# Kernel tuning notes

Hardware: AMD Instinct MI355X
Metric: run time of the kernel (lower is better)

Reference implementation:

```python
import jax, jax.numpy as jnp
import numpy as np
from jax import lax

L, H, NUM_CONVS, KSIZE = 8192, 128, 4, 7
EPS = 1e-5


def _pos_encoding(length, dim, dtype):
    pos = jnp.arange(length, dtype=jnp.float32)[:, None]
    i = jnp.arange(dim, dtype=jnp.float32)[None, :]
    angle = pos / jnp.power(10000.0, (2.0 * jnp.floor(i / 2.0)) / dim)
    pe = jnp.where((jnp.arange(dim) % 2 == 0)[None, :], jnp.sin(angle), jnp.cos(angle))
    return pe.astype(dtype)


def _layer_norm(x):
    mu = jnp.mean(x, axis=-1, keepdims=True)
    var = jnp.mean(jnp.square(x - mu), axis=-1, keepdims=True)
    return (x - mu) * lax.rsqrt(var + EPS)


def _conv1d_same(x, w, b):
    # x: [L, H]; w: [H_out, H_in, K]; b: [H_out]. SAME padding over sequence.
    lhs = x.T[None]  # [1, H, L]
    out = lax.conv_general_dilated(lhs, w, window_strides=(1,), padding='SAME',
                                   dimension_numbers=('NCH', 'OIH', 'NCH'))
    return (out[0] + b[:, None]).T  # [L, H]


def setup_inputs() -> dict:
    key = jax.random.key(0)
    ks = jax.random.split(key, 12)
    s = 0.02
    return {
        'x': jax.random.normal(ks[0], (L, H), jnp.float32),
        'conv_w': jax.random.normal(ks[1], (NUM_CONVS, H, H, KSIZE), jnp.float32) * s,
        'conv_b': jax.random.normal(ks[2], (NUM_CONVS, H), jnp.float32) * s,
        'Wq': jax.random.normal(ks[3], (H, H), jnp.float32) * s,
        'bq': jax.random.normal(ks[4], (H,), jnp.float32) * s,
        'Wk': jax.random.normal(ks[5], (H, H), jnp.float32) * s,
        'bk': jax.random.normal(ks[6], (H,), jnp.float32) * s,
        'Wv': jax.random.normal(ks[7], (H, H), jnp.float32) * s,
        'bv': jax.random.normal(ks[8], (H,), jnp.float32) * s,
        'Wff': jax.random.normal(ks[9], (H, H), jnp.float32) * s,
        'bff': jax.random.normal(ks[10], (H,), jnp.float32) * s,
    }


def reference(x, conv_w, conv_b, Wq, bq, Wk, bk, Wv, bv, Wff, bff):
    h = x + _pos_encoding(x.shape[0], x.shape[1], x.dtype)
    # conv stack: LN -> conv -> residual, repeated num_convs times
    for i in range(NUM_CONVS):
        residual = h
        h = _conv1d_same(_layer_norm(h), conv_w[i], conv_b[i]) + residual
    # self-attention (single-head as written in the source)
    residual = h
    n = _layer_norm(h)
    q = n @ Wq.T + bq
    k = n @ Wk.T + bk
    v = n @ Wv.T + bv
    scale = 1.0 / jnp.sqrt(jnp.asarray(H, h.dtype))
    attn = jax.nn.softmax((q @ k.T) * scale, axis=-1)  # [L, L]
    h = attn @ v + residual
    # feed-forward
    residual = h
    h = jax.nn.relu(_layer_norm(h) @ Wff.T + bff) + residual
    return h
```

## Files before the change

kernel.cpp:

```cpp
#include <hip/hip_runtime.h>

#define LL 8192
#define HH 128

typedef __attribute__((ext_vector_type(8))) short short8v;
typedef __attribute__((ext_vector_type(4))) short short4v;
typedef __attribute__((ext_vector_type(4))) float f32x4;
typedef __attribute__((ext_vector_type(16))) float f32x16;

__device__ inline short f2bf(float f) {
    union { float f; unsigned u; } x; x.f = f;
    unsigned r = (x.u + 0x7fffu + ((x.u >> 16) & 1u)) >> 16;
    return (short)r;
}
__device__ inline float bf2f(short s) {
    union { unsigned u; float f; } x; x.u = ((unsigned)(unsigned short)s) << 16;
    return x.f;
}

__device__ inline float fexp2(float x) {
#if defined(__has_builtin)
#if __has_builtin(__builtin_amdgcn_exp2f)
    return __builtin_amdgcn_exp2f(x);
#else
    return __expf(x * 0.6931471805599453f);
#endif
#else
    return __expf(x * 0.6931471805599453f);
#endif
}

__device__ inline unsigned pack_hi16(unsigned hi, unsigned lo) {
#if defined(__has_builtin)
#if __has_builtin(__builtin_amdgcn_perm)
    return __builtin_amdgcn_perm(hi, lo, 0x07060302u);
#endif
#endif
    return (lo >> 16) | (hi & 0xffff0000u);
}

__device__ inline void plane32swap(unsigned& a, unsigned& b) {
#if defined(__has_builtin)
#if __has_builtin(__builtin_amdgcn_permlane32_swap)
    typedef unsigned u2v __attribute__((ext_vector_type(2)));
    u2v r = __builtin_amdgcn_permlane32_swap(a, b, false, false);
    a = r[0]; b = r[1];
    return;
#endif
#endif
    asm volatile("v_permlane32_swap_b32 %0, %1" : "+v"(a), "+v"(b));
}

__device__ inline short* sAp(short* base, int row, int col) {
    int byte = (row << 8) + (col << 1);
    byte ^= (row & 7) << 4;
    return (short*)((char*)base + byte);
}

__device__ inline short8v ln_pack8(const float* rowF, int l15) {
    const float4 a = *(const float4*)&rowF[l15 * 8];
    const float4 b = *(const float4*)&rowF[l15 * 8 + 4];
    float s  = (a.x + a.y) + (a.z + a.w) + (b.x + b.y) + (b.z + b.w);
    float s2 = a.x * a.x + a.y * a.y + a.z * a.z + a.w * a.w
             + b.x * b.x + b.y * b.y + b.z * b.z + b.w * b.w;
#pragma unroll
    for (int off = 1; off <= 8; off <<= 1) {
        s  += __shfl_xor(s,  off, 64);
        s2 += __shfl_xor(s2, off, 64);
    }
    float mu = s * (1.f / 128.f);
    float var = s2 * (1.f / 128.f) - mu * mu;
    float rstd = rsqrtf(var + 1e-5f);
    short8v r;
    r[0] = f2bf((a.x - mu) * rstd);
    r[1] = f2bf((a.y - mu) * rstd);
    r[2] = f2bf((a.z - mu) * rstd);
    r[3] = f2bf((a.w - mu) * rstd);
    r[4] = f2bf((b.x - mu) * rstd);
    r[5] = f2bf((b.y - mu) * rstd);
    r[6] = f2bf((b.z - mu) * rstd);
    r[7] = f2bf((b.w - mu) * rstd);
    return r;
}

__global__ __launch_bounds__(256) void repack_all(const float* __restrict__ x,
                                                  const float* __restrict__ w,
                                                  const float* __restrict__ Wq,
                                                  const float* __restrict__ Wk,
                                                  const float* __restrict__ Wv,
                                                  const float* __restrict__ bq,
                                                  const float* __restrict__ bk,
                                                  const float* __restrict__ bv,
                                                  const float* __restrict__ Wff,
                                                  short* __restrict__ wkb,
                                                  short* __restrict__ wqkvb,
                                                  float* __restrict__ b3,
                                                  short* __restrict__ wffb,
                                                  float* __restrict__ h0) {
    const float qs = 0.08838834764831845f * 1.4426950408889634f;
    int idx = blockIdx.x * 256 + threadIdx.x;
    if (idx < 458752) {
        int k = idx % 7;
        int t = idx / 7;
        int i = t % HH; t /= HH;
        int o = t % HH;
        int lay = t / HH;
        wkb[((lay * 7 + k) * HH + o) * HH + i] = f2bf(w[idx]);
    } else {
        int j = idx - 458752;
        if (j < 49152) {
            int t = j >> 14, r = j & 16383;
            float v = (t == 0) ? Wq[r] * qs : (t == 1) ? Wk[r] : Wv[r];
            wqkvb[j] = f2bf(v);
        } else if (j < 49536) {
            int jj = j - 49152;
            b3[jj] = (jj < 128) ? bq[jj] * qs : (jj < 256) ? bk[jj - 128] : bv[jj - 256];
        } else if (j < 65920) {
            int jj = j - 49536;
            wffb[jj] = f2bf(Wff[jj]);
        } else {
            int p = j - 65920;
            if (p < 262144) {
                int g = p >> 5, c4 = (p & 31) << 2;
                float4 val = *(const float4*)&x[g * HH + c4];
                float fg = (float)g;
#pragma unroll
                for (int h = 0; h < 2; h++) {
                    int i0 = c4 + h * 2;
                    float e = (float)i0 / 128.f;
                    float ang = fg / powf(10000.f, e);
                    ((float*)&val)[h * 2]     += sinf(ang);
                    ((float*)&val)[h * 2 + 1] += cosf(ang);
                }
                *(float4*)&h0[g * HH + c4] = val;
            }
        }
    }
}

__global__ __launch_bounds__(256, 4) void conv_layer_kernel(const float* __restrict__ hin,
                                                            const short* __restrict__ wkb,
                                                            const float* __restrict__ conv_b,
                                                            float* __restrict__ hout,
                                                            int lay) {
    __shared__ float sF[22][132];
    __shared__ short sA[22 * 128];
    int tid = threadIdx.x;
    int w = tid >> 6, lane = tid & 63;
    int l15 = lane & 15, quad = lane >> 4;
    int wg = blockIdx.x;
    int m0 = ((wg & 7) * 64 + (wg >> 4)) * 16;
    int c0w = (((wg >> 3) & 1)) * 64 + w * 16;

    for (int idx = tid; idx < 22 * 32; idx += 256) {
        int r = idx >> 5, c4 = (idx & 31) << 2;
        int g = m0 - 3 + r;
        float4 val = make_float4(0.f, 0.f, 0.f, 0.f);
        if (g >= 0 && g < LL) val = *(const float4*)&hin[g * HH + c4];
        *(float4*)&sF[r][c4] = val;
    }
    __syncthreads();
#pragma unroll
    for (int rr = 0; rr < 2; rr++) {
        int row = rr * 16 + w * 4 + quad;
        if (row < 22)
            *(short8v*)sAp(sA, row, l15 * 8) = ln_pack8(&sF[row][0], l15);
    }
    __syncthreads();
    f32x4 accA = (f32x4)(0.f), accB = (f32x4)(0.f);
    const short* wl = wkb + lay * 7 * HH * HH;
    for (int k = 0; k < 7; k++) {
        const short* b0 = wl + (k * HH + c0w + l15) * HH;
#pragma unroll
        for (int ks = 0; ks < 4; ks++) {
            short8v bf = *(const short8v*)&b0[ks * 32 + quad * 8];
            short8v af = *(const short8v*)sAp(sA, l15 + k, ks * 32 + quad * 8);
            if (ks & 1) accB = __builtin_amdgcn_mfma_f32_16x16x32_bf16(af, bf, accB, 0, 0, 0);
            else        accA = __builtin_amdgcn_mfma_f32_16x16x32_bf16(af, bf, accA, 0, 0, 0);
        }
    }
    float bb = conv_b[lay * HH + c0w + l15];
#pragma unroll
    for (int r = 0; r < 4; r++) {
        int row = quad * 4 + r;
        hout[(m0 + row) * HH + c0w + l15] =
            sF[3 + row][c0w + l15] + accA[r] + accB[r] + bb;
    }
}

__global__ __launch_bounds__(256, 2) void conv_qkv_kernel(const float* __restrict__ hin,
                                                          const short* __restrict__ wkb,
                                                          const float* __restrict__ conv_b,
                                                          const short* __restrict__ wqkvb,
                                                          const float* __restrict__ b3,
                                                          float* __restrict__ hB,
                                                          short* __restrict__ qb,
                                                          short* __restrict__ kb,
                                                          short* __restrict__ vt) {
    __shared__ float sF[22][132];
    __shared__ short sA[22 * 128];
    __shared__ short sT[4][32][17];
    int tid = threadIdx.x;
    int w = tid >> 6, lane = tid & 63;
    int l15 = lane & 15, quad = lane >> 4;
    int wg = blockIdx.x;
    int m0 = ((wg & 7) * 64 + (wg >> 3)) * 16;
    int c0 = w * 32;

    for (int idx = tid; idx < 22 * 32; idx += 256) {
        int r = idx >> 5, c4 = (idx & 31) << 2;
        int g = m0 - 3 + r;
        float4 val = make_float4(0.f, 0.f, 0.f, 0.f);
        if (g >= 0 && g < LL) val = *(const float4*)&hin[g * HH + c4];
        *(float4*)&sF[r][c4] = val;
    }
    __syncthreads();
#pragma unroll
    for (int rr = 0; rr < 2; rr++) {
        int row = rr * 16 + w * 4 + quad;
        if (row < 22)
            *(short8v*)sAp(sA, row, l15 * 8) = ln_pack8(&sF[row][0], l15);
    }
    __syncthreads();
    f32x4 a0 = (f32x4)(0.f), a1 = (f32x4)(0.f);
    const short* wl = wkb + 3 * 7 * HH * HH;
    for (int k = 0; k < 7; k++) {
        const short* b0 = wl + (k * HH + c0 + l15) * HH;
        const short* b1 = b0 + 16 * HH;
#pragma unroll
        for (int ks = 0; ks < 4; ks++) {
            short8v bf0 = *(const short8v*)&b0[ks * 32 + quad * 8];
            short8v bf1 = *(const short8v*)&b1[ks * 32 + quad * 8];
            short8v af = *(const short8v*)sAp(sA, l15 + k, ks * 32 + quad * 8);
            a0 = __builtin_amdgcn_mfma_f32_16x16x32_bf16(af, bf0, a0, 0, 0, 0);
            a1 = __builtin_amdgcn_mfma_f32_16x16x32_bf16(af, bf1, a1, 0, 0, 0);
        }
    }
    float bb0 = conv_b[3 * HH + c0 + l15], bb1 = conv_b[3 * HH + c0 + 16 + l15];
#pragma unroll
    for (int r = 0; r < 4; r++) {
        int row = quad * 4 + r;
        float v0 = sF[3 + row][c0 + l15]      + a0[r] + bb0;
        float v1 = sF[3 + row][c0 + 16 + l15] + a1[r] + bb1;
        sF[3 + row][c0 + l15]      = v0;
        sF[3 + row][c0 + 16 + l15] = v1;
        hB[(m0 + row) * HH + c0 + l15]      = v0;
        hB[(m0 + row) * HH + c0 + 16 + l15] = v1;
    }
    __syncthreads();
    {
        int row = w * 4 + quad;
        *(short8v*)sAp(sA, row, l15 * 8) = ln_pack8(&sF[3 + row][0], l15);
    }
    __syncthreads();
    short8v af4[4];
#pragma unroll
    for (int ks = 0; ks < 4; ks++)
        af4[ks] = *(const short8v*)sAp(sA, l15, ks * 32 + quad * 8);

    for (int t = 0; t < 3; t++) {
        f32x4 acc0 = (f32x4)(0.f), acc1 = (f32x4)(0.f);
        const short* b0 = wqkvb + (t * 128 + c0 + l15) * HH;
        const short* b1 = b0 + 16 * HH;
#pragma unroll
        for (int ks = 0; ks < 4; ks++) {
            short8v bf0 = *(const short8v*)&b0[ks * 32 + quad * 8];
            short8v bf1 = *(const short8v*)&b1[ks * 32 + quad * 8];
            acc0 = __builtin_amdgcn_mfma_f32_16x16x32_bf16(af4[ks], bf0, acc0, 0, 0, 0);
            acc1 = __builtin_amdgcn_mfma_f32_16x16x32_bf16(af4[ks], bf1, acc1, 0, 0, 0);
        }
        float qb0 = b3[t * 128 + c0 + l15], qb1 = b3[t * 128 + c0 + 16 + l15];
        if (t < 2) {
            short* o = (t == 0) ? qb : kb;
#pragma unroll
            for (int r = 0; r < 4; r++) {
                int lr = m0 + quad * 4 + r;
                o[lr * HH + c0 + l15]      = f2bf(acc0[r] + qb0);
                o[lr * HH + c0 + 16 + l15] = f2bf(acc1[r] + qb1);
            }
        } else {
#pragma unroll
            for (int r = 0; r < 4; r++) {
                sT[w][l15][quad * 4 + r]      = f2bf(acc0[r] + qb0);
                sT[w][16 + l15][quad * 4 + r] = f2bf(acc1[r] + qb1);
            }
            asm volatile("s_waitcnt lgkmcnt(0)" ::: "memory");
#pragma unroll
            for (int cc = 0; cc < 8; cc++) {
                int col = cc * 4 + quad;
                vt[(c0 + col) * LL + m0 + l15] = sT[w][col][l15];
            }
        }
    }
}

#define FBN 64

__global__ __launch_bounds__(256, 2) void flash_mfma_kernel(const short* __restrict__ qs,
                                                            const short* __restrict__ ksrc,
                                                            const short* __restrict__ vsrc,
                                                            short* __restrict__ PO,
                                                            float* __restrict__ Pl,
                                                            int segrows) {
    __shared__ short sK[16 * 64 * 8];
    __shared__ short sV[16 * 64 * 8];

    const int tid = threadIdx.x;
    const int w = tid >> 6, lane = tid & 63;
    const int l31 = lane & 31, hi = lane >> 5;
    const int seg = blockIdx.x & 7;
    const int m0 = (blockIdx.x >> 3) * 128;
    const int jbeg = seg * segrows;
    const int nchunk = segrows >> 6;
    const int qrow = m0 + w * 32 + l31;

    short8v qf[8];
#pragma unroll
    for (int ks = 0; ks < 8; ks++)
        qf[ks] = *(const short8v*)&qs[qrow * HH + ks * 16 + hi * 8];

    float l_r = 0.f;
    f32x16 o_acc[4];
#pragma unroll
    for (int dt = 0; dt < 4; dt++) o_acc[dt] = (f32x16)(0.f);

    short8v kr[4], vr[4];
#pragma unroll
    for (int r = 0; r < 4; r++) {
        int s = w + 4 * r;
        kr[r] = *(const short8v*)&ksrc[(jbeg + (s >> 3) * 32 + l31) * HH + (s & 7) * 16 + hi * 8];
        vr[r] = *(const short8v*)&vsrc[((s >> 2) * 32 + l31) * LL + jbeg + (s & 3) * 16 + hi * 8];
    }

    for (int c = 0; c < nchunk; c++) {
        __syncthreads();
#pragma unroll
        for (int r = 0; r < 4; r++) {
            int s = w + 4 * r;
            *(short8v*)&sK[(s * 64 + lane) * 8] = kr[r];
            *(short8v*)&sV[(s * 64 + lane) * 8] = vr[r];
        }
        __syncthreads();
        if (c + 1 < nchunk) {
            const int j1 = jbeg + (c + 1) * FBN;
#pragma unroll
            for (int r = 0; r < 4; r++) {
                int s = w + 4 * r;
                kr[r] = *(const short8v*)&ksrc[(j1 + (s >> 3) * 32 + l31) * HH + (s & 7) * 16 + hi * 8];
                vr[r] = *(const short8v*)&vsrc[((s >> 2) * 32 + l31) * LL + j1 + (s & 3) * 16 + hi * 8];
            }
        }
        f32x16 s0 = (f32x16)(0.f), s1 = (f32x16)(0.f);
        __builtin_amdgcn_s_setprio(1);
#pragma unroll
        for (int ks = 0; ks < 8; ks++) {
            short8v kf0 = *(const short8v*)&sK[((ks) * 64 + lane) * 8];
            short8v kf1 = *(const short8v*)&sK[((8 + ks) * 64 + lane) * 8];
            s0 = __builtin_amdgcn_mfma_f32_32x32x16_bf16(kf0, qf[ks], s0, 0, 0, 0);
            s1 = __builtin_amdgcn_mfma_f32_32x32x16_bf16(kf1, qf[ks], s1, 0, 0, 0);
        }
        __builtin_amdgcn_s_setprio(0);
        short8v pfrag[4];
#pragma unroll
        for (int nt = 0; nt < 2; nt++) {
            const f32x16& sa = nt ? s1 : s0;
            unsigned pw[8];
#pragma unroll
            for (int m = 0; m < 8; m++) {
                float p0 = fexp2(sa[2 * m]);
                float p1 = fexp2(sa[2 * m + 1]);
                l_r += p0 + p1;
                union { float f; unsigned u; } u0, u1;
                u0.f = p0; u1.f = p1;
                pw[m] = pack_hi16(u1.u, u0.u);
            }
            plane32swap(pw[0], pw[2]);
            plane32swap(pw[1], pw[3]);
            plane32swap(pw[4], pw[6]);
            plane32swap(pw[5], pw[7]);
            union { unsigned u[4]; short8v v; } fa, fb;
            fa.u[0] = pw[0]; fa.u[1] = pw[1]; fa.u[2] = pw[2]; fa.u[3] = pw[3];
            fb.u[0] = pw[4]; fb.u[1] = pw[5]; fb.u[2] = pw[6]; fb.u[3] = pw[7];
            pfrag[nt * 2]     = fa.v;
            pfrag[nt * 2 + 1] = fb.v;
        }
        __builtin_amdgcn_s_setprio(1);
#pragma unroll
        for (int ks = 0; ks < 4; ks++)
#pragma unroll
            for (int dt = 0; dt < 4; dt++) {
                short8v vf = *(const short8v*)&sV[((dt * 4 + ks) * 64 + lane) * 8];
                o_acc[dt] = __builtin_amdgcn_mfma_f32_32x32x16_bf16(pfrag[ks], vf, o_acc[dt], 0, 0, 0);
            }
        __builtin_amdgcn_s_setprio(0);
    }
    float lsum = l_r + __shfl_xor(l_r, 32, 64);
    if (hi == 0)
        Pl[seg * LL + qrow] = lsum;
#pragma unroll
    for (int dt = 0; dt < 4; dt++)
#pragma unroll
        for (int i = 0; i < 16; i++) {
            int qr = (i & 3) + 8 * (i >> 2) + 4 * hi;
            PO[(size_t)seg * LL * HH + (size_t)(m0 + w * 32 + qr) * HH + dt * 32 + l31] =
                f2bf(o_acc[dt][i]);
        }
}

__global__ __launch_bounds__(256) void ff_kernel(const float* __restrict__ hin,
                                                 const short* __restrict__ PO,
                                                 const float* __restrict__ Pl,
                                                 const short* __restrict__ wffb,
                                                 const float* __restrict__ bff,
                                                 float* __restrict__ out,
                                                 int nsplit) {
    __shared__ float sF[16][132];
    __shared__ short sA[16 * 128];
    __shared__ float sLi[16];
    int tid = threadIdx.x;
    int w = tid >> 6, lane = tid & 63;
    int l15 = lane & 15, quad = lane >> 4;
    int wg = blockIdx.x;
    int m0 = ((wg & 7) * 64 + (wg >> 3)) * 16;

    if (tid < 16) {
        float s = 0.f;
        for (int seg = 0; seg < nsplit; seg++) s += Pl[seg * LL + m0 + tid];
        sLi[tid] = 1.f / s;
    }
    __syncthreads();
    for (int idx = tid; idx < 16 * 32; idx += 256) {
        int r = idx >> 5, c4 = (idx & 31) << 2;
        float4 hv = *(const float4*)&hin[(m0 + r) * HH + c4];
        float s0 = 0.f, s1 = 0.f, s2 = 0.f, s3 = 0.f;
        for (int seg = 0; seg < nsplit; seg++) {
            short4v pv = *(const short4v*)&PO[(size_t)seg * LL * HH + (m0 + r) * HH + c4];
            s0 += bf2f(pv[0]); s1 += bf2f(pv[1]); s2 += bf2f(pv[2]); s3 += bf2f(pv[3]);
        }
        float li = sLi[r];
        *(float4*)&sF[r][c4] = make_float4(hv.x + s0 * li, hv.y + s1 * li,
                                           hv.z + s2 * li, hv.w + s3 * li);
    }
    __syncthreads();
    {
        int row = w * 4 + quad;
        *(short8v*)sAp(sA, row, l15 * 8) = ln_pack8(&sF[row][0], l15);
    }
    __syncthreads();
    int c0 = w * 32;
    f32x4 acc0 = (f32x4)(0.f), acc1 = (f32x4)(0.f);
    const short* b0 = wffb + (c0 + l15) * HH;
    const short* b1 = b0 + 16 * HH;
#pragma unroll
    for (int ks = 0; ks < 4; ks++) {
        short8v af = *(const short8v*)sAp(sA, l15, ks * 32 + quad * 8);
        short8v bf0 = *(const short8v*)&b0[ks * 32 + quad * 8];
        short8v bf1 = *(const short8v*)&b1[ks * 32 + quad * 8];
        acc0 = __builtin_amdgcn_mfma_f32_16x16x32_bf16(af, bf0, acc0, 0, 0, 0);
        acc1 = __builtin_amdgcn_mfma_f32_16x16x32_bf16(af, bf1, acc1, 0, 0, 0);
    }
    float bb0 = bff[c0 + l15], bb1 = bff[c0 + 16 + l15];
#pragma unroll
    for (int r = 0; r < 4; r++) {
        int lr = quad * 4 + r;
        out[(m0 + lr) * HH + c0 + l15]      = fmaxf(acc0[r] + bb0, 0.f) + sF[lr][c0 + l15];
        out[(m0 + lr) * HH + c0 + 16 + l15] = fmaxf(acc1[r] + bb1, 0.f) + sF[lr][c0 + 16 + l15];
    }
}

extern "C" void kernel_launch(void* const* d_in, const int* in_sizes, int n_in,
                              void* d_out, int out_size, void* d_ws, size_t ws_size,
                              hipStream_t stream) {
    const float* x      = (const float*)d_in[0];
    const float* conv_w = (const float*)d_in[1];
    const float* conv_b = (const float*)d_in[2];
    const float* Wq = (const float*)d_in[3];
    const float* bq = (const float*)d_in[4];
    const float* Wk = (const float*)d_in[5];
    const float* bk = (const float*)d_in[6];
    const float* Wv = (const float*)d_in[7];
    const float* bv = (const float*)d_in[8];
    const float* Wff = (const float*)d_in[9];
    const float* bff = (const float*)d_in[10];
    float* out = (float*)d_out;

    char* ws = (char*)d_ws;
    const size_t MB = 1u << 20;
    float* hB   = (float*)(ws);
    short* qb   = (short*)(ws + 4 * MB);
    short* kb   = (short*)(ws + 6 * MB);
    short* vt   = (short*)(ws + 8 * MB);
    float* Pl   = (float*)(ws + 10 * MB);
    short* wffb = (short*)(ws + 10 * MB + 524288);
    short* PO   = (short*)(ws + 10 * MB + 524288 + 32768);
    short* wkb   = (short*)(ws + 16 * MB);
    short* wqkvb = (short*)(ws + 17 * MB);
    float* b3    = (float*)(ws + 17 * MB + 131072);
    float* h0    = (float*)(ws + 18 * MB);
    float* h13   = (float*)(ws + 22 * MB);
    float* h2    = h0;

    const int nsplit = 8;
    const int segrows = LL / nsplit;

    repack_all<<<3074, 256, 0, stream>>>(x, conv_w, Wq, Wk, Wv, bq, bk, bv, Wff,
                                         wkb, wqkvb, b3, wffb, h0);
    conv_layer_kernel<<<LL / 16 * 2, 256, 0, stream>>>(h0,  wkb, conv_b, h13, 0);
    conv_layer_kernel<<<LL / 16 * 2, 256, 0, stream>>>(h13, wkb, conv_b, h2,  1);
    conv_layer_kernel<<<LL / 16 * 2, 256, 0, stream>>>(h2,  wkb, conv_b, h13, 2);
    conv_qkv_kernel<<<LL / 16, 256, 0, stream>>>(h13, wkb, conv_b, wqkvb, b3,
                                                 hB, qb, kb, vt);
    flash_mfma_kernel<<<LL / 128 * nsplit, 256, 0, stream>>>(qb, kb, vt, PO, Pl, segrows);
    ff_kernel<<<LL / 16, 256, 0, stream>>>(hB, PO, Pl, wffb, bff, out, nsplit);
}
```

Before: 205.8 us.

## Fuse conv layers pairwise with halo recompute and widen attention split to sixteen

Each conv kernel now does two conv layers per block. It loads a 6-row halo and recomputes the intermediate rows for the second layer in shared memory, so the launches and global round-trips for layers 1 and 3 go away. The flash kernel's split count becomes a parameter and rises to 16 when the workspace is large enough, with segments mapped per XCD. The ff kernel is templated on the split count so its reduction loops unroll. The cost is extra MFMA work on the halo, more shared memory per block, and more partial outputs to reduce.

```diff
diff --git a/kernel.cpp b/kernel.cpp
--- a/kernel.cpp
+++ b/kernel.cpp
@@ -138,23 +138,23 @@
     }
 }
 
-__global__ __launch_bounds__(256, 4) void conv_layer_kernel(const float* __restrict__ hin,
-                                                            const short* __restrict__ wkb,
-                                                            const float* __restrict__ conv_b,
-                                                            float* __restrict__ hout,
-                                                            int lay) {
-    __shared__ float sF[22][132];
-    __shared__ short sA[22 * 128];
+__global__ __launch_bounds__(256, 2) void conv2_kernel(const float* __restrict__ hin,
+                                                       const short* __restrict__ wkb,
+                                                       const float* __restrict__ conv_b,
+                                                       float* __restrict__ hout,
+                                                       int lay0) {
+    __shared__ float sF[28][132];
+    __shared__ short sA[28 * 128];
     int tid = threadIdx.x;
     int w = tid >> 6, lane = tid & 63;
     int l15 = lane & 15, quad = lane >> 4;
     int wg = blockIdx.x;
-    int m0 = ((wg & 7) * 64 + (wg >> 4)) * 16;
-    int c0w = (((wg >> 3) & 1)) * 64 + w * 16;
-
-    for (int idx = tid; idx < 22 * 32; idx += 256) {
+    int m0 = ((wg & 7) * 64 + (wg >> 3)) * 16;
+    int c0 = w * 32;
+
+    for (int idx = tid; idx < 28 * 32; idx += 256) {
         int r = idx >> 5, c4 = (idx & 31) << 2;
-        int g = m0 - 3 + r;
+        int g = m0 - 6 + r;
         float4 val = make_float4(0.f, 0.f, 0.f, 0.f);
         if (g >= 0 && g < LL) val = *(const float4*)&hin[g * HH + c4];
         *(float4*)&sF[r][c4] = val;
@@ -163,42 +163,86 @@
 #pragma unroll
     for (int rr = 0; rr < 2; rr++) {
         int row = rr * 16 + w * 4 + quad;
-        if (row < 22)
+        if (row < 28)
             *(short8v*)sAp(sA, row, l15 * 8) = ln_pack8(&sF[row][0], l15);
     }
     __syncthreads();
-    f32x4 accA = (f32x4)(0.f), accB = (f32x4)(0.f);
-    const short* wl = wkb + lay * 7 * HH * HH;
+    const short* wl0 = wkb + lay0 * 7 * HH * HH;
+    f32x4 t0a = (f32x4)(0.f), t0b = (f32x4)(0.f);
+    f32x4 t1a = (f32x4)(0.f), t1b = (f32x4)(0.f);
     for (int k = 0; k < 7; k++) {
-        const short* b0 = wl + (k * HH + c0w + l15) * HH;
+        const short* bw0 = wl0 + (k * HH + c0 + l15) * HH;
+        const short* bw1 = bw0 + 16 * HH;
 #pragma unroll
         for (int ks = 0; ks < 4; ks++) {
-            short8v bf = *(const short8v*)&b0[ks * 32 + quad * 8];
-            short8v af = *(const short8v*)sAp(sA, l15 + k, ks * 32 + quad * 8);
-            if (ks & 1) accB = __builtin_amdgcn_mfma_f32_16x16x32_bf16(af, bf, accB, 0, 0, 0);
-            else        accA = __builtin_amdgcn_mfma_f32_16x16x32_bf16(af, bf, accA, 0, 0, 0);
-        }
-    }
-    float bb = conv_b[lay * HH + c0w + l15];
+            short8v bf0 = *(const short8v*)&bw0[ks * 32 + quad * 8];
+            short8v bf1 = *(const short8v*)&bw1[ks * 32 + quad * 8];
+            short8v a0 = *(const short8v*)sAp(sA, l15 + k, ks * 32 + quad * 8);
+            short8v a1 = *(const short8v*)sAp(sA, 6 + l15 + k, ks * 32 + quad * 8);
+            t0a = __builtin_amdgcn_mfma_f32_16x16x32_bf16(a0, bf0, t0a, 0, 0, 0);
+            t0b = __builtin_amdgcn_mfma_f32_16x16x32_bf16(a0, bf1, t0b, 0, 0, 0);
+            t1a = __builtin_amdgcn_mfma_f32_16x16x32_bf16(a1, bf0, t1a, 0, 0, 0);
+            t1b = __builtin_amdgcn_mfma_f32_16x16x32_bf16(a1, bf1, t1b, 0, 0, 0);
+        }
+    }
+    float b0l = conv_b[lay0 * HH + c0 + l15], b0h = conv_b[lay0 * HH + c0 + 16 + l15];
 #pragma unroll
     for (int r = 0; r < 4; r++) {
-        int row = quad * 4 + r;
-        hout[(m0 + row) * HH + c0w + l15] =
-            sF[3 + row][c0w + l15] + accA[r] + accB[r] + bb;
-    }
-}
-
-__global__ __launch_bounds__(256, 2) void conv_qkv_kernel(const float* __restrict__ hin,
-                                                          const short* __restrict__ wkb,
-                                                          const float* __restrict__ conv_b,
-                                                          const short* __restrict__ wqkvb,
-                                                          const float* __restrict__ b3,
-                                                          float* __restrict__ hB,
-                                                          short* __restrict__ qb,
-                                                          short* __restrict__ kb,
-                                                          short* __restrict__ vt) {
-    __shared__ float sF[22][132];
-    __shared__ short sA[22 * 128];
+        int rr0 = quad * 4 + r;
+        sF[3 + rr0][c0 + l15]      += t0a[r] + b0l;
+        sF[3 + rr0][c0 + 16 + l15] += t0b[r] + b0h;
+        if (rr0 >= 10) {
+            sF[9 + rr0][c0 + l15]      += t1a[r] + b0l;
+            sF[9 + rr0][c0 + 16 + l15] += t1b[r] + b0h;
+        }
+    }
+    __syncthreads();
+#pragma unroll
+    for (int rr = 0; rr < 2; rr++) {
+        int row = 3 + rr * 16 + w * 4 + quad;
+        if (row < 25) {
+            short8v pk = ln_pack8(&sF[row][0], l15);
+            int g = m0 - 6 + row;
+            if (g < 0 || g >= LL) pk = (short8v)(short)0;
+            *(short8v*)sAp(sA, row, l15 * 8) = pk;
+        }
+    }
+    __syncthreads();
+    const short* wl1 = wkb + (lay0 + 1) * 7 * HH * HH;
+    f32x4 ca = (f32x4)(0.f), cb = (f32x4)(0.f);
+    for (int k = 0; k < 7; k++) {
+        const short* bw0 = wl1 + (k * HH + c0 + l15) * HH;
+        const short* bw1 = bw0 + 16 * HH;
+#pragma unroll
+        for (int ks = 0; ks < 4; ks++) {
+            short8v bf0 = *(const short8v*)&bw0[ks * 32 + quad * 8];
+            short8v bf1 = *(const short8v*)&bw1[ks * 32 + quad * 8];
+            short8v af = *(const short8v*)sAp(sA, 3 + l15 + k, ks * 32 + quad * 8);
+            ca = __builtin_amdgcn_mfma_f32_16x16x32_bf16(af, bf0, ca, 0, 0, 0);
+            cb = __builtin_amdgcn_mfma_f32_16x16x32_bf16(af, bf1, cb, 0, 0, 0);
+        }
+    }
+    float b1l = conv_b[(lay0 + 1) * HH + c0 + l15], b1h = conv_b[(lay0 + 1) * HH + c0 + 16 + l15];
+#pragma unroll
+    for (int r = 0; r < 4; r++) {
+        int i = 6 + quad * 4 + r;
+        int g = m0 + quad * 4 + r;
+        hout[g * HH + c0 + l15]      = sF[i][c0 + l15]      + ca[r] + b1l;
+        hout[g * HH + c0 + 16 + l15] = sF[i][c0 + 16 + l15] + cb[r] + b1h;
+    }
+}
+
+__global__ __launch_bounds__(256, 2) void conv2_qkv_kernel(const float* __restrict__ hin,
+                                                           const short* __restrict__ wkb,
+                                                           const float* __restrict__ conv_b,
+                                                           const short* __restrict__ wqkvb,
+                                                           const float* __restrict__ b3,
+                                                           float* __restrict__ hB,
+                                                           short* __restrict__ qb,
+                                                           short* __restrict__ kb,
+                                                           short* __restrict__ vt) {
+    __shared__ float sF[28][132];
+    __shared__ short sA[28 * 128];
     __shared__ short sT[4][32][17];
     int tid = threadIdx.x;
     int w = tid >> 6, lane = tid & 63;
@@ -207,9 +251,9 @@
     int m0 = ((wg & 7) * 64 + (wg >> 3)) * 16;
     int c0 = w * 32;
 
-    for (int idx = tid; idx < 22 * 32; idx += 256) {
+    for (int idx = tid; idx < 28 * 32; idx += 256) {
         int r = idx >> 5, c4 = (idx & 31) << 2;
-        int g = m0 - 3 + r;
+        int g = m0 - 6 + r;
         float4 val = make_float4(0.f, 0.f, 0.f, 0.f);
         if (g >= 0 && g < LL) val = *(const float4*)&hin[g * HH + c4];
         *(float4*)&sF[r][c4] = val;
@@ -218,39 +262,81 @@
 #pragma unroll
     for (int rr = 0; rr < 2; rr++) {
         int row = rr * 16 + w * 4 + quad;
-        if (row < 22)
+        if (row < 28)
             *(short8v*)sAp(sA, row, l15 * 8) = ln_pack8(&sF[row][0], l15);
     }
     __syncthreads();
-    f32x4 a0 = (f32x4)(0.f), a1 = (f32x4)(0.f);
-    const short* wl = wkb + 3 * 7 * HH * HH;
+    const short* wl2 = wkb + 2 * 7 * HH * HH;
+    f32x4 t0a = (f32x4)(0.f), t0b = (f32x4)(0.f);
+    f32x4 t1a = (f32x4)(0.f), t1b = (f32x4)(0.f);
     for (int k = 0; k < 7; k++) {
-        const short* b0 = wl + (k * HH + c0 + l15) * HH;
-        const short* b1 = b0 + 16 * HH;
+        const short* bw0 = wl2 + (k * HH + c0 + l15) * HH;
+        const short* bw1 = bw0 + 16 * HH;
 #pragma unroll
         for (int ks = 0; ks < 4; ks++) {
-            short8v bf0 = *(const short8v*)&b0[ks * 32 + quad * 8];
-            short8v bf1 = *(const short8v*)&b1[ks * 32 + quad * 8];
-            short8v af = *(const short8v*)sAp(sA, l15 + k, ks * 32 + quad * 8);
-            a0 = __builtin_amdgcn_mfma_f32_16x16x32_bf16(af, bf0, a0, 0, 0, 0);
-            a1 = __builtin_amdgcn_mfma_f32_16x16x32_bf16(af, bf1, a1, 0, 0, 0);
-        }
-    }
-    float bb0 = conv_b[3 * HH + c0 + l15], bb1 = conv_b[3 * HH + c0 + 16 + l15];
+            short8v bf0 = *(const short8v*)&bw0[ks * 32 + quad * 8];
+            short8v bf1 = *(const short8v*)&bw1[ks * 32 + quad * 8];
+            short8v a0 = *(const short8v*)sAp(sA, l15 + k, ks * 32 + quad * 8);
+            short8v a1 = *(const short8v*)sAp(sA, 6 + l15 + k, ks * 32 + quad * 8);
+            t0a = __builtin_amdgcn_mfma_f32_16x16x32_bf16(a0, bf0, t0a, 0, 0, 0);
+            t0b = __builtin_amdgcn_mfma_f32_16x16x32_bf16(a0, bf1, t0b, 0, 0, 0);
+            t1a = __builtin_amdgcn_mfma_f32_16x16x32_bf16(a1, bf0, t1a, 0, 0, 0);
+            t1b = __builtin_amdgcn_mfma_f32_16x16x32_bf16(a1, bf1, t1b, 0, 0, 0);
+        }
+    }
+    float b2l = conv_b[2 * HH + c0 + l15], b2h = conv_b[2 * HH + c0 + 16 + l15];
 #pragma unroll
     for (int r = 0; r < 4; r++) {
-        int row = quad * 4 + r;
-        float v0 = sF[3 + row][c0 + l15]      + a0[r] + bb0;
-        float v1 = sF[3 + row][c0 + 16 + l15] + a1[r] + bb1;
-        sF[3 + row][c0 + l15]      = v0;
-        sF[3 + row][c0 + 16 + l15] = v1;
-        hB[(m0 + row) * HH + c0 + l15]      = v0;
-        hB[(m0 + row) * HH + c0 + 16 + l15] = v1;
+        int rr0 = quad * 4 + r;
+        sF[3 + rr0][c0 + l15]      += t0a[r] + b2l;
+        sF[3 + rr0][c0 + 16 + l15] += t0b[r] + b2h;
+        if (rr0 >= 10) {
+            sF[9 + rr0][c0 + l15]      += t1a[r] + b2l;
+            sF[9 + rr0][c0 + 16 + l15] += t1b[r] + b2h;
+        }
+    }
+    __syncthreads();
+#pragma unroll
+    for (int rr = 0; rr < 2; rr++) {
+        int row = 3 + rr * 16 + w * 4 + quad;
+        if (row < 25) {
+            short8v pk = ln_pack8(&sF[row][0], l15);
+            int g = m0 - 6 + row;
+            if (g < 0 || g >= LL) pk = (short8v)(short)0;
+            *(short8v*)sAp(sA, row, l15 * 8) = pk;
+        }
+    }
+    __syncthreads();
+    const short* wl3 = wkb + 3 * 7 * HH * HH;
+    f32x4 ca = (f32x4)(0.f), cb = (f32x4)(0.f);
+    for (int k = 0; k < 7; k++) {
+        const short* bw0 = wl3 + (k * HH + c0 + l15) * HH;
+        const short* bw1 = bw0 + 16 * HH;
+#pragma unroll
+        for (int ks = 0; ks < 4; ks++) {
+            short8v bf0 = *(const short8v*)&bw0[ks * 32 + quad * 8];
+            short8v bf1 = *(const short8v*)&bw1[ks * 32 + quad * 8];
+            short8v af = *(const short8v*)sAp(sA, 3 + l15 + k, ks * 32 + quad * 8);
+            ca = __builtin_amdgcn_mfma_f32_16x16x32_bf16(af, bf0, ca, 0, 0, 0);
+            cb = __builtin_amdgcn_mfma_f32_16x16x32_bf16(af, bf1, cb, 0, 0, 0);
+        }
+    }
+    float b3l = conv_b[3 * HH + c0 + l15], b3h = conv_b[3 * HH + c0 + 16 + l15];
+#pragma unroll
+    for (int r = 0; r < 4; r++) {
+        int i = 6 + quad * 4 + r;
+        int g = m0 + quad * 4 + r;
+        float v0 = sF[i][c0 + l15]      + ca[r] + b3l;
+        float v1 = sF[i][c0 + 16 + l15] + cb[r] + b3h;
+        sF[i][c0 + l15]      = v0;
+        sF[i][c0 + 16 + l15] = v1;
+        hB[g * HH + c0 + l15]      = v0;
+        hB[g * HH + c0 + 16 + l15] = v1;
     }
     __syncthreads();
     {
         int row = w * 4 + quad;
-        *(short8v*)sAp(sA, row, l15 * 8) = ln_pack8(&sF[3 + row][0], l15);
+        *(short8v*)sAp(sA, row, l15 * 8) = ln_pack8(&sF[6 + row][0], l15);
     }
     __syncthreads();
     short8v af4[4];
@@ -301,15 +387,20 @@
                                                             const short* __restrict__ vsrc,
                                                             short* __restrict__ PO,
                                                             float* __restrict__ Pl,
-                                                            int segrows) {
+                                                            int segrows, int nsplit) {
     __shared__ short sK[16 * 64 * 8];
     __shared__ short sV[16 * 64 * 8];
 
     const int tid = threadIdx.x;
     const int w = tid >> 6, lane = tid & 63;
     const int l31 = lane & 31, hi = lane >> 5;
-    const int seg = blockIdx.x & 7;
-    const int m0 = (blockIdx.x >> 3) * 128;
+    const int bid = blockIdx.x;
+    const int xcd = bid & 7;
+    const int t = bid >> 3;
+    const int spx = nsplit >> 3;
+    const int sh = spx >> 1;
+    const int seg = xcd * spx + (t & (spx - 1));
+    const int m0 = (t >> sh) * 128;
     const int jbeg = seg * segrows;
     const int nchunk = segrows >> 6;
     const int qrow = m0 + w * 32 + l31;
@@ -407,13 +498,13 @@
         }
 }
 
+template<int NSPLIT>
 __global__ __launch_bounds__(256) void ff_kernel(const float* __restrict__ hin,
                                                  const short* __restrict__ PO,
                                                  const float* __restrict__ Pl,
                                                  const short* __restrict__ wffb,
                                                  const float* __restrict__ bff,
-                                                 float* __restrict__ out,
-                                                 int nsplit) {
+                                                 float* __restrict__ out) {
     __shared__ float sF[16][132];
     __shared__ short sA[16 * 128];
     __shared__ float sLi[16];
@@ -425,7 +516,8 @@
 
     if (tid < 16) {
         float s = 0.f;
-        for (int seg = 0; seg < nsplit; seg++) s += Pl[seg * LL + m0 + tid];
+#pragma unroll
+        for (int seg = 0; seg < NSPLIT; seg++) s += Pl[seg * LL + m0 + tid];
         sLi[tid] = 1.f / s;
     }
     __syncthreads();
@@ -433,7 +525,8 @@
         int r = idx >> 5, c4 = (idx & 31) << 2;
         float4 hv = *(const float4*)&hin[(m0 + r) * HH + c4];
         float s0 = 0.f, s1 = 0.f, s2 = 0.f, s3 = 0.f;
-        for (int seg = 0; seg < nsplit; seg++) {
+#pragma unroll
+        for (int seg = 0; seg < NSPLIT; seg++) {
             short4v pv = *(const short4v*)&PO[(size_t)seg * LL * HH + (m0 + r) * HH + c4];
             s0 += bf2f(pv[0]); s1 += bf2f(pv[1]); s2 += bf2f(pv[2]); s3 += bf2f(pv[3]);
         }
@@ -497,19 +590,20 @@
     short* wqkvb = (short*)(ws + 17 * MB);
     float* b3    = (float*)(ws + 17 * MB + 131072);
     float* h0    = (float*)(ws + 18 * MB);
-    float* h13   = (float*)(ws + 22 * MB);
-    float* h2    = h0;
-
-    const int nsplit = 8;
+    float* h2    = (float*)(ws + 22 * MB);
+
+    const int nsplit = (ws_size >= (size_t)44 * MB) ? 16 : 8;
     const int segrows = LL / nsplit;
 
     repack_all<<<3074, 256, 0, stream>>>(x, conv_w, Wq, Wk, Wv, bq, bk, bv, Wff,
                                          wkb, wqkvb, b3, wffb, h0);
-    conv_layer_kernel<<<LL / 16 * 2, 256, 0, stream>>>(h0,  wkb, conv_b, h13, 0);
-    conv_layer_kernel<<<LL / 16 * 2, 256, 0, stream>>>(h13, wkb, conv_b, h2,  1);
-    conv_layer_kernel<<<LL / 16 * 2, 256, 0, stream>>>(h2,  wkb, conv_b, h13, 2);
-    conv_qkv_kernel<<<LL / 16, 256, 0, stream>>>(h13, wkb, conv_b, wqkvb, b3,
-                                                 hB, qb, kb, vt);
-    flash_mfma_kernel<<<LL / 128 * nsplit, 256, 0, stream>>>(qb, kb, vt, PO, Pl, segrows);
-    ff_kernel<<<LL / 16, 256, 0, stream>>>(hB, PO, Pl, wffb, bff, out, nsplit);
-}
+    conv2_kernel<<<LL / 16, 256, 0, stream>>>(h0, wkb, conv_b, h2, 0);
+    conv2_qkv_kernel<<<LL / 16, 256, 0, stream>>>(h2, wkb, conv_b, wqkvb, b3,
+                                                  hB, qb, kb, vt);
+    flash_mfma_kernel<<<LL / 128 * nsplit, 256, 0, stream>>>(qb, kb, vt, PO, Pl,
+                                                             segrows, nsplit);
+    if (nsplit == 16)
+        ff_kernel<16><<<LL / 16, 256, 0, stream>>>(hB, PO, Pl, wffb, bff, out);
+    else
+        ff_kernel<8><<<LL / 16, 256, 0, stream>>>(hB, PO, Pl, wffb, bff, out);
+}
```

Result: no change. 202.9 us (-1.4%).

## Fuse four conv layers and QKV projection into one halo-recompute kernel

Applied to the files above, without the earlier changes.

Replaces the three per-layer conv launches plus the conv+QKV kernel with a single kernel. Each block loads a 40-row tile with a 12-row halo and recomputes the shrinking halo through all four conv layers in shared memory. This removes three launches and the global round-trips of the intermediate activations, but adds redundant conv MFMA work on halo rows and uses more LDS per block. The positional-encoding sin/cos moves to exp2 plus range-reduced fast __sinf/__cosf, and the split count becomes a compile-time constant so its loops can be unrolled.

```diff
diff --git a/kernel.cpp b/kernel.cpp
--- a/kernel.cpp
+++ b/kernel.cpp
@@ -128,9 +128,11 @@
                 for (int h = 0; h < 2; h++) {
                     int i0 = c4 + h * 2;
                     float e = (float)i0 / 128.f;
-                    float ang = fg / powf(10000.f, e);
-                    ((float*)&val)[h * 2]     += sinf(ang);
-                    ((float*)&val)[h * 2 + 1] += cosf(ang);
+                    float rev = fg * fexp2(e * -13.287712379549449f - 2.651496129472319f);
+                    rev -= floorf(rev);
+                    float ang = rev * 6.283185307179586f;
+                    ((float*)&val)[h * 2]     += __sinf(ang);
+                    ((float*)&val)[h * 2 + 1] += __cosf(ang);
                 }
                 *(float4*)&h0[g * HH + c4] = val;
             }
@@ -138,67 +140,17 @@
     }
 }
 
-__global__ __launch_bounds__(256, 4) void conv_layer_kernel(const float* __restrict__ hin,
-                                                            const short* __restrict__ wkb,
-                                                            const float* __restrict__ conv_b,
-                                                            float* __restrict__ hout,
-                                                            int lay) {
-    __shared__ float sF[22][132];
-    __shared__ short sA[22 * 128];
-    int tid = threadIdx.x;
-    int w = tid >> 6, lane = tid & 63;
-    int l15 = lane & 15, quad = lane >> 4;
-    int wg = blockIdx.x;
-    int m0 = ((wg & 7) * 64 + (wg >> 4)) * 16;
-    int c0w = (((wg >> 3) & 1)) * 64 + w * 16;
-
-    for (int idx = tid; idx < 22 * 32; idx += 256) {
-        int r = idx >> 5, c4 = (idx & 31) << 2;
-        int g = m0 - 3 + r;
-        float4 val = make_float4(0.f, 0.f, 0.f, 0.f);
-        if (g >= 0 && g < LL) val = *(const float4*)&hin[g * HH + c4];
-        *(float4*)&sF[r][c4] = val;
-    }
-    __syncthreads();
-#pragma unroll
-    for (int rr = 0; rr < 2; rr++) {
-        int row = rr * 16 + w * 4 + quad;
-        if (row < 22)
-            *(short8v*)sAp(sA, row, l15 * 8) = ln_pack8(&sF[row][0], l15);
-    }
-    __syncthreads();
-    f32x4 accA = (f32x4)(0.f), accB = (f32x4)(0.f);
-    const short* wl = wkb + lay * 7 * HH * HH;
-    for (int k = 0; k < 7; k++) {
-        const short* b0 = wl + (k * HH + c0w + l15) * HH;
-#pragma unroll
-        for (int ks = 0; ks < 4; ks++) {
-            short8v bf = *(const short8v*)&b0[ks * 32 + quad * 8];
-            short8v af = *(const short8v*)sAp(sA, l15 + k, ks * 32 + quad * 8);
-            if (ks & 1) accB = __builtin_amdgcn_mfma_f32_16x16x32_bf16(af, bf, accB, 0, 0, 0);
-            else        accA = __builtin_amdgcn_mfma_f32_16x16x32_bf16(af, bf, accA, 0, 0, 0);
-        }
-    }
-    float bb = conv_b[lay * HH + c0w + l15];
-#pragma unroll
-    for (int r = 0; r < 4; r++) {
-        int row = quad * 4 + r;
-        hout[(m0 + row) * HH + c0w + l15] =
-            sF[3 + row][c0w + l15] + accA[r] + accB[r] + bb;
-    }
-}
-
-__global__ __launch_bounds__(256, 2) void conv_qkv_kernel(const float* __restrict__ hin,
-                                                          const short* __restrict__ wkb,
-                                                          const float* __restrict__ conv_b,
-                                                          const short* __restrict__ wqkvb,
-                                                          const float* __restrict__ b3,
-                                                          float* __restrict__ hB,
-                                                          short* __restrict__ qb,
-                                                          short* __restrict__ kb,
-                                                          short* __restrict__ vt) {
-    __shared__ float sF[22][132];
-    __shared__ short sA[22 * 128];
+__global__ __launch_bounds__(256, 2) void conv4_qkv_kernel(const float* __restrict__ h0,
+                                                           const short* __restrict__ wkb,
+                                                           const float* __restrict__ conv_b,
+                                                           const short* __restrict__ wqkvb,
+                                                           const float* __restrict__ b3,
+                                                           float* __restrict__ hB,
+                                                           short* __restrict__ qb,
+                                                           short* __restrict__ kb,
+                                                           short* __restrict__ vt) {
+    __shared__ float sF[40][132];
+    __shared__ short sA[54 * 128];
     __shared__ short sT[4][32][17];
     int tid = threadIdx.x;
     int w = tid >> 6, lane = tid & 63;
@@ -207,50 +159,159 @@
     int m0 = ((wg & 7) * 64 + (wg >> 3)) * 16;
     int c0 = w * 32;
 
-    for (int idx = tid; idx < 22 * 32; idx += 256) {
+    for (int idx = tid; idx < 40 * 32; idx += 256) {
         int r = idx >> 5, c4 = (idx & 31) << 2;
-        int g = m0 - 3 + r;
+        int g = m0 - 12 + r;
         float4 val = make_float4(0.f, 0.f, 0.f, 0.f);
-        if (g >= 0 && g < LL) val = *(const float4*)&hin[g * HH + c4];
+        if (g >= 0 && g < LL) val = *(const float4*)&h0[g * HH + c4];
         *(float4*)&sF[r][c4] = val;
     }
     __syncthreads();
 #pragma unroll
+    for (int rr = 0; rr < 3; rr++) {
+        int row = rr * 16 + w * 4 + quad;
+        if (row < 40)
+            *(short8v*)sAp(sA, row, l15 * 8) = ln_pack8(&sF[row][0], l15);
+    }
+    __syncthreads();
+
+    const float* cb = conv_b;
+#define CONV_TILE(wl, B, aca, acb)                                                  \
+    {                                                                               \
+        for (int k = 0; k < 7; k++) {                                               \
+            const short* bw0 = (wl) + (k * HH + c0 + l15) * HH;                     \
+            const short* bw1 = bw0 + 16 * HH;                                       \
+            _Pragma("unroll")                                                       \
+            for (int ks = 0; ks < 4; ks++) {                                        \
+                short8v bf0 = *(const short8v*)&bw0[ks * 32 + quad * 8];            \
+                short8v bf1 = *(const short8v*)&bw1[ks * 32 + quad * 8];            \
+                short8v af = *(const short8v*)sAp(sA, (B) - 3 + l15 + k,            \
+                                                  ks * 32 + quad * 8);              \
+                aca = __builtin_amdgcn_mfma_f32_16x16x32_bf16(af, bf0, aca, 0, 0, 0); \
+                acb = __builtin_amdgcn_mfma_f32_16x16x32_bf16(af, bf1, acb, 0, 0, 0); \
+            }                                                                       \
+        }                                                                           \
+    }
+
+    {
+        const short* wl = wkb + 0 * 7 * HH * HH;
+        f32x4 a0a = (f32x4)(0.f), a0b = (f32x4)(0.f);
+        f32x4 a1a = (f32x4)(0.f), a1b = (f32x4)(0.f);
+        f32x4 a2a = (f32x4)(0.f), a2b = (f32x4)(0.f);
+        CONV_TILE(wl, 3,  a0a, a0b);
+        CONV_TILE(wl, 19, a1a, a1b);
+        CONV_TILE(wl, 35, a2a, a2b);
+        float bl = cb[0 * HH + c0 + l15], bh = cb[0 * HH + c0 + 16 + l15];
+#pragma unroll
+        for (int r = 0; r < 4; r++) {
+            int rr0 = quad * 4 + r;
+            sF[3 + rr0][c0 + l15]       += a0a[r] + bl;
+            sF[3 + rr0][c0 + 16 + l15]  += a0b[r] + bh;
+            sF[19 + rr0][c0 + l15]      += a1a[r] + bl;
+            sF[19 + rr0][c0 + 16 + l15] += a1b[r] + bh;
+            if (rr0 < 2) {
+                sF[35 + rr0][c0 + l15]      += a2a[r] + bl;
+                sF[35 + rr0][c0 + 16 + l15] += a2b[r] + bh;
+            }
+        }
+    }
+    __syncthreads();
+#pragma unroll
+    for (int rr = 0; rr < 3; rr++) {
+        int row = 3 + rr * 16 + w * 4 + quad;
+        if (row < 37) {
+            short8v pk = ln_pack8(&sF[row][0], l15);
+            int g = m0 - 12 + row;
+            if (g < 0 || g >= LL) pk = (short8v)(short)0;
+            *(short8v*)sAp(sA, row, l15 * 8) = pk;
+        }
+    }
+    __syncthreads();
+
+    {
+        const short* wl = wkb + 1 * 7 * HH * HH;
+        f32x4 a0a = (f32x4)(0.f), a0b = (f32x4)(0.f);
+        f32x4 a1a = (f32x4)(0.f), a1b = (f32x4)(0.f);
+        CONV_TILE(wl, 6,  a0a, a0b);
+        CONV_TILE(wl, 22, a1a, a1b);
+        float bl = cb[1 * HH + c0 + l15], bh = cb[1 * HH + c0 + 16 + l15];
+#pragma unroll
+        for (int r = 0; r < 4; r++) {
+            int rr0 = quad * 4 + r;
+            sF[6 + rr0][c0 + l15]      += a0a[r] + bl;
+            sF[6 + rr0][c0 + 16 + l15] += a0b[r] + bh;
+            if (rr0 < 12) {
+                sF[22 + rr0][c0 + l15]      += a1a[r] + bl;
+                sF[22 + rr0][c0 + 16 + l15] += a1b[r] + bh;
+            }
+        }
+    }
+    __syncthreads();
+#pragma unroll
     for (int rr = 0; rr < 2; rr++) {
-        int row = rr * 16 + w * 4 + quad;
-        if (row < 22)
-            *(short8v*)sAp(sA, row, l15 * 8) = ln_pack8(&sF[row][0], l15);
-    }
-    __syncthreads();
-    f32x4 a0 = (f32x4)(0.f), a1 = (f32x4)(0.f);
-    const short* wl = wkb + 3 * 7 * HH * HH;
-    for (int k = 0; k < 7; k++) {
-        const short* b0 = wl + (k * HH + c0 + l15) * HH;
-        const short* b1 = b0 + 16 * HH;
-#pragma unroll
-        for (int ks = 0; ks < 4; ks++) {
-            short8v bf0 = *(const short8v*)&b0[ks * 32 + quad * 8];
-            short8v bf1 = *(const short8v*)&b1[ks * 32 + quad * 8];
-            short8v af = *(const short8v*)sAp(sA, l15 + k, ks * 32 + quad * 8);
-            a0 = __builtin_amdgcn_mfma_f32_16x16x32_bf16(af, bf0, a0, 0, 0, 0);
-            a1 = __builtin_amdgcn_mfma_f32_16x16x32_bf16(af, bf1, a1, 0, 0, 0);
-        }
-    }
-    float bb0 = conv_b[3 * HH + c0 + l15], bb1 = conv_b[3 * HH + c0 + 16 + l15];
-#pragma unroll
-    for (int r = 0; r < 4; r++) {
-        int row = quad * 4 + r;
-        float v0 = sF[3 + row][c0 + l15]      + a0[r] + bb0;
-        float v1 = sF[3 + row][c0 + 16 + l15] + a1[r] + bb1;
-        sF[3 + row][c0 + l15]      = v0;
-        sF[3 + row][c0 + 16 + l15] = v1;
-        hB[(m0 + row) * HH + c0 + l15]      = v0;
-        hB[(m0 + row) * HH + c0 + 16 + l15] = v1;
-    }
-    __syncthreads();
+        int row = 6 + rr * 16 + w * 4 + quad;
+        if (row < 34) {
+            short8v pk = ln_pack8(&sF[row][0], l15);
+            int g = m0 - 12 + row;
+            if (g < 0 || g >= LL) pk = (short8v)(short)0;
+            *(short8v*)sAp(sA, row, l15 * 8) = pk;
+        }
+    }
+    __syncthreads();
+
+    {
+        const short* wl = wkb + 2 * 7 * HH * HH;
+        f32x4 a0a = (f32x4)(0.f), a0b = (f32x4)(0.f);
+        f32x4 a1a = (f32x4)(0.f), a1b = (f32x4)(0.f);
+        CONV_TILE(wl, 9,  a0a, a0b);
+        CONV_TILE(wl, 25, a1a, a1b);
+        float bl = cb[2 * HH + c0 + l15], bh = cb[2 * HH + c0 + 16 + l15];
+#pragma unroll
+        for (int r = 0; r < 4; r++) {
+            int rr0 = quad * 4 + r;
+            sF[9 + rr0][c0 + l15]      += a0a[r] + bl;
+            sF[9 + rr0][c0 + 16 + l15] += a0b[r] + bh;
+            if (rr0 < 6) {
+                sF[25 + rr0][c0 + l15]      += a1a[r] + bl;
+                sF[25 + rr0][c0 + 16 + l15] += a1b[r] + bh;
+            }
+        }
+    }
+    __syncthreads();
+#pragma unroll
+    for (int rr = 0; rr < 2; rr++) {
+        int row = 9 + rr * 16 + w * 4 + quad;
+        if (row < 31) {
+            short8v pk = ln_pack8(&sF[row][0], l15);
+            int g = m0 - 12 + row;
+            if (g < 0 || g >= LL) pk = (short8v)(short)0;
+            *(short8v*)sAp(sA, row, l15 * 8) = pk;
+        }
+    }
+    __syncthreads();
+
+    {
+        const short* wl = wkb + 3 * 7 * HH * HH;
+        f32x4 a0a = (f32x4)(0.f), a0b = (f32x4)(0.f);
+        CONV_TILE(wl, 12, a0a, a0b);
+        float bl = cb[3 * HH + c0 + l15], bh = cb[3 * HH + c0 + 16 + l15];
+#pragma unroll
+        for (int r = 0; r < 4; r++) {
+            int rr0 = quad * 4 + r;
+            int g = m0 + rr0;
+            float v0 = sF[12 + rr0][c0 + l15]      + a0a[r] + bl;
+            float v1 = sF[12 + rr0][c0 + 16 + l15] + a0b[r] + bh;
+            sF[12 + rr0][c0 + l15]      = v0;
+            sF[12 + rr0][c0 + 16 + l15] = v1;
+            hB[g * HH + c0 + l15]      = v0;
+            hB[g * HH + c0 + 16 + l15] = v1;
+        }
+    }
+    __syncthreads();
+#undef CONV_TILE
     {
         int row = w * 4 + quad;
-        *(short8v*)sAp(sA, row, l15 * 8) = ln_pack8(&sF[3 + row][0], l15);
+        *(short8v*)sAp(sA, row, l15 * 8) = ln_pack8(&sF[12 + row][0], l15);
     }
     __syncthreads();
     short8v af4[4];
@@ -295,13 +356,14 @@
 }
 
 #define FBN 64
+#define NSPLIT 8
+#define SEGROWS (LL / NSPLIT)
 
 __global__ __launch_bounds__(256, 2) void flash_mfma_kernel(const short* __restrict__ qs,
                                                             const short* __restrict__ ksrc,
                                                             const short* __restrict__ vsrc,
                                                             short* __restrict__ PO,
-                                                            float* __restrict__ Pl,
-                                                            int segrows) {
+                                                            float* __restrict__ Pl) {
     __shared__ short sK[16 * 64 * 8];
     __shared__ short sV[16 * 64 * 8];
 
@@ -310,8 +372,8 @@
     const int l31 = lane & 31, hi = lane >> 5;
     const int seg = blockIdx.x & 7;
     const int m0 = (blockIdx.x >> 3) * 128;
-    const int jbeg = seg * segrows;
-    const int nchunk = segrows >> 6;
+    const int jbeg = seg * SEGROWS;
+    const int nchunk = SEGROWS >> 6;
     const int qrow = m0 + w * 32 + l31;
 
     short8v qf[8];
@@ -412,8 +474,7 @@
                                                  const float* __restrict__ Pl,
                                                  const short* __restrict__ wffb,
                                                  const float* __restrict__ bff,
-                                                 float* __restrict__ out,
-                                                 int nsplit) {
+                                                 float* __restrict__ out) {
     __shared__ float sF[16][132];
     __shared__ short sA[16 * 128];
     __shared__ float sLi[16];
@@ -425,7 +486,8 @@
 
     if (tid < 16) {
         float s = 0.f;
-        for (int seg = 0; seg < nsplit; seg++) s += Pl[seg * LL + m0 + tid];
+#pragma unroll
+        for (int seg = 0; seg < NSPLIT; seg++) s += Pl[seg * LL + m0 + tid];
         sLi[tid] = 1.f / s;
     }
     __syncthreads();
@@ -433,7 +495,8 @@
         int r = idx >> 5, c4 = (idx & 31) << 2;
         float4 hv = *(const float4*)&hin[(m0 + r) * HH + c4];
         float s0 = 0.f, s1 = 0.f, s2 = 0.f, s3 = 0.f;
-        for (int seg = 0; seg < nsplit; seg++) {
+#pragma unroll
+        for (int seg = 0; seg < NSPLIT; seg++) {
             short4v pv = *(const short4v*)&PO[(size_t)seg * LL * HH + (m0 + r) * HH + c4];
             s0 += bf2f(pv[0]); s1 += bf2f(pv[1]); s2 += bf2f(pv[2]); s3 += bf2f(pv[3]);
         }
@@ -497,19 +560,11 @@
     short* wqkvb = (short*)(ws + 17 * MB);
     float* b3    = (float*)(ws + 17 * MB + 131072);
     float* h0    = (float*)(ws + 18 * MB);
-    float* h13   = (float*)(ws + 22 * MB);
-    float* h2    = h0;
-
-    const int nsplit = 8;
-    const int segrows = LL / nsplit;
 
     repack_all<<<3074, 256, 0, stream>>>(x, conv_w, Wq, Wk, Wv, bq, bk, bv, Wff,
                                          wkb, wqkvb, b3, wffb, h0);
-    conv_layer_kernel<<<LL / 16 * 2, 256, 0, stream>>>(h0,  wkb, conv_b, h13, 0);
-    conv_layer_kernel<<<LL / 16 * 2, 256, 0, stream>>>(h13, wkb, conv_b, h2,  1);
-    conv_layer_kernel<<<LL / 16 * 2, 256, 0, stream>>>(h2,  wkb, conv_b, h13, 2);
-    conv_qkv_kernel<<<LL / 16, 256, 0, stream>>>(h13, wkb, conv_b, wqkvb, b3,
-                                                 hB, qb, kb, vt);
-    flash_mfma_kernel<<<LL / 128 * nsplit, 256, 0, stream>>>(qb, kb, vt, PO, Pl, segrows);
-    ff_kernel<<<LL / 16, 256, 0, stream>>>(hB, PO, Pl, wffb, bff, out, nsplit);
-}
+    conv4_qkv_kernel<<<LL / 16, 256, 0, stream>>>(h0, wkb, conv_b, wqkvb, b3,
+                                                  hB, qb, kb, vt);
+    flash_mfma_kernel<<<LL / 128 * NSPLIT, 256, 0, stream>>>(qb, kb, vt, PO, Pl);
+    ff_kernel<<<LL / 16, 256, 0, stream>>>(hB, PO, Pl, wffb, bff, out);
+}
```

New measurement: 195.0 us. 5.3% less time.
